# Performance work log

Hardware: AMD Instinct MI355X
Metric: run time of the kernel (lower is better)

The kernel has to match this reference:

```python
import jax, jax.numpy as jnp
import numpy as np

H = 1024      # hidden_dim
NH = 16       # num_heads
HD = H // NH  # head_dim
FF = 4 * H
EPS = 1e-5

def _ln(x, g, b):
    m = jnp.mean(x, axis=-1, keepdims=True)
    v = jnp.var(x, axis=-1, keepdims=True)
    return (x - m) * jax.lax.rsqrt(v + EPS) * g + b

def setup_inputs() -> dict:
    key = jax.random.key(0)
    ks = jax.random.split(key, 12)
    s = 1.0 / np.sqrt(H)
    inp = {
        'x': jax.random.normal(ks[0], (2, 2048, H), dtype=jnp.float32),
        'Wq': jax.random.normal(ks[1], (H, H), dtype=jnp.float32) * s,
        'bq': jnp.zeros((H,), dtype=jnp.float32),
        'Wk': jax.random.normal(ks[2], (H, H), dtype=jnp.float32) * s,
        'bk': jnp.zeros((H,), dtype=jnp.float32),
        'Wv': jax.random.normal(ks[3], (H, H), dtype=jnp.float32) * s,
        'bv': jnp.zeros((H,), dtype=jnp.float32),
        'Wo': jax.random.normal(ks[4], (H, H), dtype=jnp.float32) * s,
        'bo': jnp.zeros((H,), dtype=jnp.float32),
        'g1': jnp.ones((H,), dtype=jnp.float32),
        'b1': jnp.zeros((H,), dtype=jnp.float32),
        'W1': jax.random.normal(ks[5], (H, FF), dtype=jnp.float32) * s,
        'bf1': jnp.zeros((FF,), dtype=jnp.float32),
        'W2': jax.random.normal(ks[6], (FF, H), dtype=jnp.float32) * (1.0 / np.sqrt(FF)),
        'bf2': jnp.zeros((H,), dtype=jnp.float32),
        'g2': jnp.ones((H,), dtype=jnp.float32),
        'b2': jnp.zeros((H,), dtype=jnp.float32),
    }
    return inp

def reference(x, Wq, bq, Wk, bk, Wv, bv, Wo, bo, g1, b1, W1, bf1, W2, bf2, g2, b2):
    B, S, _ = x.shape
    residual = x
    xn = _ln(x, g1, b1)
    # [B,S,H] -> [B,NH,S,HD]
    def split_heads(t):
        return t.reshape(B, S, NH, HD).transpose(0, 2, 1, 3)
    q = split_heads(xn @ Wq + bq)
    k = split_heads(xn @ Wk + bk)
    v = split_heads(xn @ Wv + bv)
    scores = jnp.einsum('bhqd,bhkd->bhqk', q, k) / np.sqrt(HD).astype(np.float32)
    attn = jax.nn.softmax(scores, axis=-1)
    ctx = jnp.einsum('bhqk,bhkd->bhqd', attn, v)
    ctx = ctx.transpose(0, 2, 1, 3).reshape(B, S, H)
    out = ctx @ Wo + bo + residual
    residual = out
    on = _ln(out, g2, b2)
    out = jax.nn.relu(on @ W1 + bf1) @ W2 + bf2 + residual
    return out
```

## Files before the change

### kernel.cpp

```cpp
#include <hip/hip_runtime.h>
#include <hip/hip_bf16.h>

constexpr int HDIM = 1024;
constexpr int NHEAD = 16;
constexpr int FFDIM = 4096;
constexpr int SEQLEN = 2048;
constexpr int NTOK = 4096;

typedef __bf16 bf16x8 __attribute__((ext_vector_type(8)));
typedef float f32x4 __attribute__((ext_vector_type(4)));
typedef short s16x4 __attribute__((ext_vector_type(4)));

union U16x8 {
    s16x4 h[2];
    bf16x8 v;
    int4 raw;
    unsigned u[4];
    short s[8];
};

__device__ __forceinline__ short f2bf(float f) {
    union { float f; unsigned u; } c;
    c.f = f;
    return (short)((c.u + 0x8000u) >> 16);
}

__device__ __forceinline__ unsigned cvtpk(float a, float b) {
    __hip_bfloat162 h = __float22bfloat162_rn(float2{a, b});
    return *reinterpret_cast<unsigned*>(&h);
}

__device__ __forceinline__ float exp2_raw(float x) {
    float r;
    asm("v_exp_f32 %0, %1" : "=v"(r) : "v"(x));
    return r;
}

template <int N>
__device__ __forceinline__ void wait_vmcnt() {
    if constexpr (N == 0) asm volatile("s_waitcnt vmcnt(0)" ::: "memory");
    else if constexpr (N == 6) asm volatile("s_waitcnt vmcnt(6)" ::: "memory");
    else static_assert(N == 0 || N == 6, "unsupported vmcnt");
}
__device__ __forceinline__ void barrier_fence() {
    __builtin_amdgcn_s_barrier();
    asm volatile("" ::: "memory");
}

__device__ __forceinline__ void gload16(const void* gsrc, void* lds) {
    __builtin_amdgcn_global_load_lds(
        (const __attribute__((address_space(1))) unsigned int*)gsrc,
        (__attribute__((address_space(3))) unsigned int*)lds, 16, 0, 0);
}


constexpr float QSCALE = 0.18033688011112042f;

__global__ __launch_bounds__(256)
void wconv_all(const float* __restrict__ Wq, const float* __restrict__ Wk,
               const float* __restrict__ Wv, const float* __restrict__ Wo,
               const float* __restrict__ W1, const float* __restrict__ W2,
               short* __restrict__ qkvT, short* __restrict__ WoT,
               short* __restrict__ W1T, short* __restrict__ W2T) {
    int i = blockIdx.x;
    const float* W;
    short* WT;
    int K, N, bx, by;
    if (i < 2048) {
        const int w = i >> 9;
        i &= 511;
        K = HDIM; N = HDIM; bx = i & 3; by = i >> 2;
        W = w == 0 ? Wq : w == 1 ? Wk : w == 2 ? Wv : Wo;
        WT = w == 3 ? WoT : qkvT + (size_t)w * HDIM * HDIM;
    } else if (i < 4096) {
        i -= 2048;
        K = HDIM; N = FFDIM; bx = i & 15; by = i >> 4;
        W = W1; WT = W1T;
    } else {
        i -= 4096;
        K = FFDIM; N = HDIM; bx = i & 3; by = i >> 2;
        W = W2; WT = W2T;
    }
    const int n = bx * 256 + threadIdx.x;
    const int g = by >> 2, fc = by & 3;
    const int k0 = g * 32 + fc * 4;
    float a[4], c[4];
#pragma unroll
    for (int j = 0; j < 4; ++j) a[j] = W[(size_t)(k0 + j) * N + n];
#pragma unroll
    for (int j = 0; j < 4; ++j) c[j] = W[(size_t)(k0 + 16 + j) * N + n];
    U16x8 u;
    u.u[0] = cvtpk(a[0], a[1]);
    u.u[1] = cvtpk(a[2], a[3]);
    u.u[2] = cvtpk(c[0], c[1]);
    u.u[3] = cvtpk(c[2], c[3]);
    *(int4*)(WT + (size_t)n * K + by * 8) = u.raw;
}

__global__ __launch_bounds__(256)
void ln_bf16(const float* __restrict__ x, const float* __restrict__ g,
             const float* __restrict__ b, short* __restrict__ out) {
    const int row = blockIdx.x, t = threadIdx.x;
    const float* xr = x + (size_t)row * HDIM;
    float4 v = *(const float4*)&xr[t * 4];
    float s = v.x + v.y + v.z + v.w;
    float ss = v.x * v.x + v.y * v.y + v.z * v.z + v.w * v.w;
#pragma unroll
    for (int o = 32; o > 0; o >>= 1) {
        s += __shfl_down(s, o);
        ss += __shfl_down(ss, o);
    }
    __shared__ float red[8];
    const int wv = t >> 6, ln = t & 63;
    if (ln == 0) { red[wv] = s; red[4 + wv] = ss; }
    __syncthreads();
    s = red[0] + red[1] + red[2] + red[3];
    ss = red[4] + red[5] + red[6] + red[7];
    const float mean = s * (1.0f / HDIM);
    const float var = ss * (1.0f / HDIM) - mean * mean;
    const float rstd = rsqrtf(var + 1e-5f);
    float4 gv = *(const float4*)&g[t * 4];
    float4 bv = *(const float4*)&b[t * 4];
    union { s16x4 h4; uint2 u2; } pk;
    pk.u2.x = cvtpk((v.x - mean) * rstd * gv.x + bv.x, (v.y - mean) * rstd * gv.y + bv.y);
    pk.u2.y = cvtpk((v.z - mean) * rstd * gv.z + bv.z, (v.w - mean) * rstd * gv.w + bv.w);
    const int kk = (t * 4) & 31;
    const int dst = ((t * 4) & ~31) + ((kk & 15) >> 2) * 8 + (kk >> 4) * 4;
    *(s16x4*)&out[(size_t)row * HDIM + dst] = pk.h4;
}

template <int BM, int BN, int MODE, int PIPE>
__global__ __launch_bounds__(256, PIPE ? 2 : (((BM + BN) == 256) ? 3 : 4))
void gemm_bf16(const short* __restrict__ A, const short* __restrict__ BT,
               const float* __restrict__ bias, const float* __restrict__ resid,
               void* __restrict__ outp, int M, int N, int K,
               const float* __restrict__ bias2, const float* __restrict__ bias3,
               void* __restrict__ out3) {
    constexpr int MI = BM / 32, NJ = BN / 32;
    constexpr int NSEG = (BM + BN) / 16;
    constexpr int PW = NSEG / 4;
    constexpr int BUFS = (BM + BN) * 32;
    constexpr int NBUF = PIPE ? 6 : 2;
    static_assert(!PIPE || (BM + BN) == 192, "PIPE=1 tuned for PW=3 (vmcnt 6)");
    __shared__ short LdsF[NBUF * BUFS];
    const int tid = threadIdx.x;
    const int lane = tid & 63, wave = tid >> 6;
    const int wm = wave >> 1, wn = wave & 1;
    const int l15 = lane & 15, lg = lane >> 4;
    const int lsw = lg ^ ((l15 >> 1) & 3);
    const int m0 = blockIdx.x * BM, n0 = blockIdx.y * BN;
    const int nk = K >> 5;
    const int sr = lane >> 2;
    const int sc8 = (((lane & 3) ^ ((sr >> 1) & 3))) * 8;

    auto stage = [&](int buf, int kt) {
#pragma unroll
        for (int p = 0; p < PW; ++p) {
            const int s = wave + p * 4;
            const short* src = (s < BM / 16)
                ? A + (size_t)(m0 + s * 16 + sr) * K + kt * 32 + sc8
                : BT + (size_t)(n0 + (s - BM / 16) * 16 + sr) * K + kt * 32 + sc8;
            const int off = __builtin_amdgcn_readfirstlane(buf * BUFS * 2 + s * 1024);
            gload16(src, (char*)LdsF + off);
        }
    };
    auto compute = [&](int buf, f32x4 (&acc)[MI][NJ]) {
        bf16x8 af[MI], bfr[NJ];
#pragma unroll
        for (int i = 0; i < MI; ++i)
            af[i] = *(const bf16x8*)&LdsF[buf * BUFS +
                                          (wm * (BM / 2) + i * 16 + l15) * 32 + lsw * 8];
#pragma unroll
        for (int j = 0; j < NJ; ++j)
            bfr[j] = *(const bf16x8*)&LdsF[buf * BUFS +
                                           (BM + wn * (BN / 2) + j * 16 + l15) * 32 + lsw * 8];
#pragma unroll
        for (int i = 0; i < MI; ++i)
#pragma unroll
            for (int j = 0; j < NJ; ++j)
                acc[i][j] = __builtin_amdgcn_mfma_f32_16x16x32_bf16(af[i], bfr[j], acc[i][j], 0, 0, 0);
    };

    f32x4 acc[MI][NJ] = {};
    if constexpr (PIPE == 0) {
        stage(0, 0);
        for (int kt = 0; kt < nk; ++kt) {
            const int buf = kt & 1;
            __syncthreads();
            if (kt + 1 < nk) stage(buf ^ 1, kt + 1);
            compute(buf, acc);
        }
    } else {
        stage(0, 0); stage(1, 1); stage(2, 2); stage(3, 3);
        const int np = nk >> 1;
        int pc = 0, ps = 2;
        for (int t = 0; t < np; ++t) {
            if (t + 1 < np) wait_vmcnt<6>();
            else wait_vmcnt<0>();
            barrier_fence();
            if (t + 2 < np) {
                stage(ps * 2, 2 * t + 4);
                stage(ps * 2 + 1, 2 * t + 5);
            }
            compute(pc * 2, acc);
            compute(pc * 2 + 1, acc);
            pc = (pc == 2) ? 0 : pc + 1;
            ps = (ps == 2) ? 0 : ps + 1;
        }
    }

    const int rbase = m0 + wm * (BM / 2);
    const int cbase = n0 + wn * (BN / 2);
    if constexpr (MODE == 0) {
#pragma unroll
        for (int i = 0; i < MI; ++i)
#pragma unroll
            for (int j = 0; j < NJ; ++j) {
                const int c = cbase + j * 16 + l15;
                const float bv = bias[c];
#pragma unroll
                for (int ii = 0; ii < 4; ++ii) {
                    const int r = rbase + i * 16 + lg * 4 + ii;
                    const size_t idx = (size_t)r * N + c;
                    ((float*)outp)[idx] = acc[i][j][ii] + bv + resid[idx];
                }
            }
    } else if constexpr (MODE == 1) {
#pragma unroll
        for (int i = 0; i < MI; ++i)
#pragma unroll
            for (int j = 0; j < NJ; ++j) {
                const int c = cbase + j * 16 + l15;
                const float bv = bias[c];
                const int cp = (c & ~31) | ((l15 >> 2) * 8 + (j & 1) * 4 + (l15 & 3));
#pragma unroll
                for (int ii = 0; ii < 4; ++ii) {
                    const int r = rbase + i * 16 + lg * 4 + ii;
                    float v = acc[i][j][ii] + bv;
                    v = v > 0.0f ? v : 0.0f;
                    ((short*)outp)[(size_t)r * N + cp] = f2bf(v);
                }
            }
    } else {
        const int which = n0 >> 10;
        if (which < 2) {
            const float* bb = which == 0 ? bias : bias2;
            const float qs = which == 0 ? QSCALE : 1.0f;
            short* QKp = (short*)outp;
#pragma unroll
            for (int i = 0; i < MI; ++i)
#pragma unroll
                for (int j = 0; j < NJ; ++j) {
                    const int c = cbase + j * 16 + l15;
                    const float bv = bb[c & 1023];
                    const int cp = (c & ~31) | ((l15 >> 2) * 8 + (j & 1) * 4 + (l15 & 3));
#pragma unroll
                    for (int ii = 0; ii < 4; ++ii) {
                        const int r = rbase + i * 16 + lg * 4 + ii;
                        QKp[(size_t)r * 2048 + cp] = f2bf((acc[i][j][ii] + bv) * qs);
                    }
                }
        } else {
            short* VTp = (short*)out3;
#pragma unroll
            for (int j = 0; j < NJ; ++j) {
                const int c = cbase + j * 16 + l15;
                const int cc = c - 2048;
                const int hh = cc >> 6, dd = cc & 63;
                const float bv = bias3[cc];
#pragma unroll
                for (int i = 0; i < MI; ++i) {
                    const int r0 = rbase + i * 16 + lg * 4;
                    const int bb_ = r0 >> 11;
                    const int s0 = r0 & (SEQLEN - 1);
                    const int sbase = (s0 & ~31) + lg * 8 + (i & 1) * 4;
                    union { s16x4 h4; uint2 u2; } pk;
                    pk.u2.x = cvtpk(acc[i][j][0] + bv, acc[i][j][1] + bv);
                    pk.u2.y = cvtpk(acc[i][j][2] + bv, acc[i][j][3] + bv);
                    *(s16x4*)&VTp[(((size_t)(bb_ * NHEAD + hh)) * 64 + dd) * SEQLEN + sbase] = pk.h4;
                }
            }
        }
    }
}

__global__ __launch_bounds__(256, 4)
void attn_fwd(const short* __restrict__ QK, const short* __restrict__ VT,
              short* __restrict__ ctx) {
    __shared__ short KlF[2 * 4096];
    __shared__ short VlF[2 * 4096];
    const int tid = threadIdx.x, lane = tid & 63, wave = tid >> 6;
    const int l15 = lane & 15, lg = lane >> 4;
    const int lsw = lg ^ ((l15 >> 1) & 3);
    const int bid = blockIdx.x;
    const int xcd = bid & 7, li = bid >> 3;
    const int bh = xcd * 4 + (li >> 5);
    const int qt = li & 31;
    const int b = bh >> 4, h = bh & 15;
    const size_t tokbase = (size_t)b * SEQLEN;
    const int sr = lane >> 2;
    const int sc8 = (((lane & 3) ^ ((sr >> 1) & 3))) * 8;

    const short* kp = QK + (tokbase + wave * 16 + sr) * 2048 + 1024 + h * 64 + sc8;
    const short* vp = VT + ((size_t)bh * 64 + wave * 16 + sr) * SEQLEN + sc8;

    auto stage = [&](int buf) {
        const int off = __builtin_amdgcn_readfirstlane(buf * 8192 + wave * 1024);
        gload16(kp, (char*)KlF + off);
        gload16(kp + 32, (char*)KlF + off + 4096);
        gload16(vp, (char*)VlF + off);
        gload16(vp + 32, (char*)VlF + off + 4096);
    };

    const short* qp = QK + (tokbase + qt * 64 + wave * 16 + l15) * 2048 + h * 64;
    bf16x8 qf[2];
    qf[0] = *(const bf16x8*)(qp + lg * 8);
    qf[1] = *(const bf16x8*)(qp + 32 + lg * 8);

    U16x8 uo;
#pragma unroll
    for (int j = 0; j < 8; ++j) uo.s[j] = 0x3F80;
    const bf16x8 onesv = uo.v;

    f32x4 o[4] = {};
    f32x4 Lacc = {};
    stage(0);
    for (int kt = 0; kt < SEQLEN / 64; ++kt) {
        const int buf = kt & 1;
        __syncthreads();
        if (kt + 1 < SEQLEN / 64) {
            kp += 64 * 2048;
            vp += 64;
            stage(buf ^ 1);
        }

        f32x4 sc[4];
        __builtin_amdgcn_s_setprio(1);
#pragma unroll
        for (int j = 0; j < 4; ++j) {
            bf16x8 kf0 = *(const bf16x8*)&KlF[buf * 4096 + (j * 16 + l15) * 32 + lsw * 8];
            bf16x8 kf1 = *(const bf16x8*)&KlF[buf * 4096 + 2048 + (j * 16 + l15) * 32 + lsw * 8];
            f32x4 z = {};
            z = __builtin_amdgcn_mfma_f32_16x16x32_bf16(kf0, qf[0], z, 0, 0, 0);
            sc[j] = __builtin_amdgcn_mfma_f32_16x16x32_bf16(kf1, qf[1], z, 0, 0, 0);
        }
        __builtin_amdgcn_s_setprio(0);

        U16x8 u0, u1;
        u0.u[0] = cvtpk(exp2_raw(sc[0][0]), exp2_raw(sc[0][1]));
        u0.u[1] = cvtpk(exp2_raw(sc[0][2]), exp2_raw(sc[0][3]));
        u0.u[2] = cvtpk(exp2_raw(sc[1][0]), exp2_raw(sc[1][1]));
        u0.u[3] = cvtpk(exp2_raw(sc[1][2]), exp2_raw(sc[1][3]));
        u1.u[0] = cvtpk(exp2_raw(sc[2][0]), exp2_raw(sc[2][1]));
        u1.u[1] = cvtpk(exp2_raw(sc[2][2]), exp2_raw(sc[2][3]));
        u1.u[2] = cvtpk(exp2_raw(sc[3][0]), exp2_raw(sc[3][1]));
        u1.u[3] = cvtpk(exp2_raw(sc[3][2]), exp2_raw(sc[3][3]));

        __builtin_amdgcn_s_setprio(1);
#pragma unroll
        for (int ks = 0; ks < 2; ++ks) {
            const bf16x8 pf = ks == 0 ? u0.v : u1.v;
            Lacc = __builtin_amdgcn_mfma_f32_16x16x32_bf16(onesv, pf, Lacc, 0, 0, 0);
#pragma unroll
            for (int fd = 0; fd < 4; ++fd) {
                bf16x8 vf = *(const bf16x8*)&VlF[buf * 4096 + ks * 2048 + (fd * 16 + l15) * 32 + lsw * 8];
                o[fd] = __builtin_amdgcn_mfma_f32_16x16x32_bf16(vf, pf, o[fd], 0, 0, 0);
            }
        }
        __builtin_amdgcn_s_setprio(0);
    }

    const float rl = 1.0f / Lacc[0];
    const int qrow = qt * 64 + wave * 16 + l15;
    short* crow = ctx + (tokbase + qrow) * HDIM + h * 64;
#pragma unroll
    for (int fd = 0; fd < 4; ++fd) {
        s16x4 v4;
#pragma unroll
        for (int ii = 0; ii < 4; ++ii) v4[ii] = f2bf(o[fd][ii] * rl);
        *(s16x4*)(crow + (fd >> 1) * 32 + lg * 8 + (fd & 1) * 4) = v4;
    }
}

extern "C" void kernel_launch(void* const* d_in, const int* in_sizes, int n_in,
                              void* d_out, int out_size, void* d_ws, size_t ws_size,
                              hipStream_t stream) {
    const float* x  = (const float*)d_in[0];
    const float* Wq = (const float*)d_in[1];
    const float* bq = (const float*)d_in[2];
    const float* Wk = (const float*)d_in[3];
    const float* bk = (const float*)d_in[4];
    const float* Wv = (const float*)d_in[5];
    const float* bv = (const float*)d_in[6];
    const float* Wo = (const float*)d_in[7];
    const float* bo = (const float*)d_in[8];
    const float* g1 = (const float*)d_in[9];
    const float* b1 = (const float*)d_in[10];
    const float* W1 = (const float*)d_in[11];
    const float* bf1 = (const float*)d_in[12];
    const float* W2 = (const float*)d_in[13];
    const float* bf2 = (const float*)d_in[14];
    const float* g2 = (const float*)d_in[15];
    const float* b2 = (const float*)d_in[16];

    char* ws = (char*)d_ws;
    const size_t MB = 1024 * 1024;
    short* qkvT = (short*)(ws + 0 * MB);
    short* WoT  = (short*)(ws + 6 * MB);
    short* W1T  = (short*)(ws + 8 * MB);
    short* W2T  = (short*)(ws + 16 * MB);
    short* xn   = (short*)(ws + 24 * MB);
    short* QKb  = (short*)(ws + 32 * MB);
    short* VTb  = (short*)(ws + 48 * MB);
    short* ctx  = (short*)(ws + 56 * MB);
    float* out1 = (float*)(ws + 64 * MB);
    short* h1   = (short*)(ws + 32 * MB);

    wconv_all<<<6144, 256, 0, stream>>>(Wq, Wk, Wv, Wo, W1, W2, qkvT, WoT, W1T, W2T);

    ln_bf16<<<NTOK, 256, 0, stream>>>(x, g1, b1, xn);

    gemm_bf16<128, 128, 2, 0><<<dim3(NTOK / 128, 3072 / 128), 256, 0, stream>>>(
        xn, qkvT, bq, nullptr, QKb, NTOK, 3072, HDIM, bk, bv, VTb);

    attn_fwd<<<1024, 256, 0, stream>>>(QKb, VTb, ctx);

    gemm_bf16<128, 64, 0, 1><<<dim3(NTOK / 128, HDIM / 64), 256, 0, stream>>>(
        ctx, WoT, bo, x, out1, NTOK, HDIM, HDIM, nullptr, nullptr, nullptr);

    ln_bf16<<<NTOK, 256, 0, stream>>>(out1, g2, b2, xn);

    gemm_bf16<128, 128, 1, 0><<<dim3(NTOK / 128, FFDIM / 128), 256, 0, stream>>>(
        xn, W1T, bf1, nullptr, h1, NTOK, FFDIM, HDIM, nullptr, nullptr, nullptr);

    gemm_bf16<128, 64, 0, 1><<<dim3(NTOK / 128, HDIM / 64), 256, 0, stream>>>(
        h1, W2T, bf2, out1, (float*)d_out, NTOK, HDIM, FFDIM, nullptr, nullptr, nullptr);
}
```

Before: 222.2 us.

## Add 4-buffer prefetch pipeline for 128x128 GEMMs and wave-per-row LayerNorm

Adds a PIPE=2 mode for the 128x128 GEMMs (QKV and FFN1). It uses 4 LDS buffers and keeps two K-steps in flight with vmcnt(8) waits, replacing plain double buffering so global loads overlap MFMA work better. It also rewrites LayerNorm so one wave handles one row with xor shuffles, dropping the shared-memory reduction and block barrier. The cost is double the LDS per block for those GEMMs, which, together with launch bounds lowered to 2, may reduce occupancy, plus an extra barrier per iteration.

```diff
diff --git a/kernel.cpp b/kernel.cpp
--- a/kernel.cpp
+++ b/kernel.cpp
@@ -40,7 +40,8 @@
 __device__ __forceinline__ void wait_vmcnt() {
     if constexpr (N == 0) asm volatile("s_waitcnt vmcnt(0)" ::: "memory");
     else if constexpr (N == 6) asm volatile("s_waitcnt vmcnt(6)" ::: "memory");
-    else static_assert(N == 0 || N == 6, "unsupported vmcnt");
+    else if constexpr (N == 8) asm volatile("s_waitcnt vmcnt(8)" ::: "memory");
+    else static_assert(N == 0 || N == 6 || N == 8, "unsupported vmcnt");
 }
 __device__ __forceinline__ void barrier_fence() {
     __builtin_amdgcn_s_barrier();
@@ -100,33 +101,40 @@
 __global__ __launch_bounds__(256)
 void ln_bf16(const float* __restrict__ x, const float* __restrict__ g,
              const float* __restrict__ b, short* __restrict__ out) {
-    const int row = blockIdx.x, t = threadIdx.x;
+    const int wave = threadIdx.x >> 6, lane = threadIdx.x & 63;
+    const int row = blockIdx.x * 4 + wave;
     const float* xr = x + (size_t)row * HDIM;
-    float4 v = *(const float4*)&xr[t * 4];
-    float s = v.x + v.y + v.z + v.w;
-    float ss = v.x * v.x + v.y * v.y + v.z * v.z + v.w * v.w;
+    float4 v[4];
+    float s = 0.0f, ss = 0.0f;
+#pragma unroll
+    for (int i = 0; i < 4; ++i) {
+        v[i] = *(const float4*)&xr[i * 256 + lane * 4];
+        s += v[i].x + v[i].y + v[i].z + v[i].w;
+        ss += v[i].x * v[i].x + v[i].y * v[i].y + v[i].z * v[i].z + v[i].w * v[i].w;
+    }
 #pragma unroll
     for (int o = 32; o > 0; o >>= 1) {
-        s += __shfl_down(s, o);
-        ss += __shfl_down(ss, o);
-    }
-    __shared__ float red[8];
-    const int wv = t >> 6, ln = t & 63;
-    if (ln == 0) { red[wv] = s; red[4 + wv] = ss; }
-    __syncthreads();
-    s = red[0] + red[1] + red[2] + red[3];
-    ss = red[4] + red[5] + red[6] + red[7];
+        s += __shfl_xor(s, o);
+        ss += __shfl_xor(ss, o);
+    }
     const float mean = s * (1.0f / HDIM);
     const float var = ss * (1.0f / HDIM) - mean * mean;
     const float rstd = rsqrtf(var + 1e-5f);
-    float4 gv = *(const float4*)&g[t * 4];
-    float4 bv = *(const float4*)&b[t * 4];
-    union { s16x4 h4; uint2 u2; } pk;
-    pk.u2.x = cvtpk((v.x - mean) * rstd * gv.x + bv.x, (v.y - mean) * rstd * gv.y + bv.y);
-    pk.u2.y = cvtpk((v.z - mean) * rstd * gv.z + bv.z, (v.w - mean) * rstd * gv.w + bv.w);
-    const int kk = (t * 4) & 31;
-    const int dst = ((t * 4) & ~31) + ((kk & 15) >> 2) * 8 + (kk >> 4) * 4;
-    *(s16x4*)&out[(size_t)row * HDIM + dst] = pk.h4;
+    short* orow = out + (size_t)row * HDIM;
+#pragma unroll
+    for (int i = 0; i < 4; ++i) {
+        const int c = i * 256 + lane * 4;
+        float4 gv = *(const float4*)&g[c];
+        float4 bv = *(const float4*)&b[c];
+        union { s16x4 h4; uint2 u2; } pk;
+        pk.u2.x = cvtpk((v[i].x - mean) * rstd * gv.x + bv.x,
+                        (v[i].y - mean) * rstd * gv.y + bv.y);
+        pk.u2.y = cvtpk((v[i].z - mean) * rstd * gv.z + bv.z,
+                        (v[i].w - mean) * rstd * gv.w + bv.w);
+        const int kk = c & 31;
+        const int dst = (c & ~31) + ((kk & 15) >> 2) * 8 + (kk >> 4) * 4;
+        *(s16x4*)&orow[dst] = pk.h4;
+    }
 }
 
 template <int BM, int BN, int MODE, int PIPE>
@@ -140,8 +148,9 @@
     constexpr int NSEG = (BM + BN) / 16;
     constexpr int PW = NSEG / 4;
     constexpr int BUFS = (BM + BN) * 32;
-    constexpr int NBUF = PIPE ? 6 : 2;
-    static_assert(!PIPE || (BM + BN) == 192, "PIPE=1 tuned for PW=3 (vmcnt 6)");
+    constexpr int NBUF = (PIPE == 1) ? 6 : (PIPE == 2) ? 4 : 2;
+    static_assert(PIPE != 1 || (BM + BN) == 192, "PIPE=1 tuned for PW=3 (vmcnt 6)");
+    static_assert(PIPE != 2 || (BM + BN) == 256, "PIPE=2 tuned for PW=4 (vmcnt 8)");
     __shared__ short LdsF[NBUF * BUFS];
     const int tid = threadIdx.x;
     const int lane = tid & 63, wave = tid >> 6;
@@ -190,7 +199,7 @@
             if (kt + 1 < nk) stage(buf ^ 1, kt + 1);
             compute(buf, acc);
         }
-    } else {
+    } else if constexpr (PIPE == 1) {
         stage(0, 0); stage(1, 1); stage(2, 2); stage(3, 3);
         const int np = nk >> 1;
         int pc = 0, ps = 2;
@@ -206,6 +215,22 @@
             compute(pc * 2 + 1, acc);
             pc = (pc == 2) ? 0 : pc + 1;
             ps = (ps == 2) ? 0 : ps + 1;
+        }
+    } else {
+        stage(0, 0); stage(1, 1); stage(2, 2); stage(3, 3);
+        const int np = nk >> 1;
+        for (int t = 0; t < np; ++t) {
+            const int pb = (t & 1) * 2;
+            if (t + 1 < np) wait_vmcnt<8>();
+            else wait_vmcnt<0>();
+            barrier_fence();
+            compute(pb, acc);
+            compute(pb + 1, acc);
+            if (t + 2 < np) {
+                barrier_fence();
+                stage(pb, 2 * t + 4);
+                stage(pb + 1, 2 * t + 5);
+            }
         }
     }
 
@@ -418,9 +443,9 @@
 
     wconv_all<<<6144, 256, 0, stream>>>(Wq, Wk, Wv, Wo, W1, W2, qkvT, WoT, W1T, W2T);
 
-    ln_bf16<<<NTOK, 256, 0, stream>>>(x, g1, b1, xn);
-
-    gemm_bf16<128, 128, 2, 0><<<dim3(NTOK / 128, 3072 / 128), 256, 0, stream>>>(
+    ln_bf16<<<NTOK / 4, 256, 0, stream>>>(x, g1, b1, xn);
+
+    gemm_bf16<128, 128, 2, 2><<<dim3(NTOK / 128, 3072 / 128), 256, 0, stream>>>(
         xn, qkvT, bq, nullptr, QKb, NTOK, 3072, HDIM, bk, bv, VTb);
 
     attn_fwd<<<1024, 256, 0, stream>>>(QKb, VTb, ctx);
@@ -428,9 +453,9 @@
     gemm_bf16<128, 64, 0, 1><<<dim3(NTOK / 128, HDIM / 64), 256, 0, stream>>>(
         ctx, WoT, bo, x, out1, NTOK, HDIM, HDIM, nullptr, nullptr, nullptr);
 
-    ln_bf16<<<NTOK, 256, 0, stream>>>(out1, g2, b2, xn);
-
-    gemm_bf16<128, 128, 1, 0><<<dim3(NTOK / 128, FFDIM / 128), 256, 0, stream>>>(
+    ln_bf16<<<NTOK / 4, 256, 0, stream>>>(out1, g2, b2, xn);
+
+    gemm_bf16<128, 128, 1, 2><<<dim3(NTOK / 128, FFDIM / 128), 256, 0, stream>>>(
         xn, W1T, bf1, nullptr, h1, NTOK, FFDIM, HDIM, nullptr, nullptr, nullptr);
 
     gemm_bf16<128, 64, 0, 1><<<dim3(NTOK / 128, HDIM / 64), 256, 0, stream>>>(
```

Result: no change. 218.1 us (-1.9%).
